# Optimization experiments

Measured on AMD Instinct MI355X. Metric: run time of the kernel, lower is better.

The kernel has to match this reference:

```python
import jax, jax.numpy as jnp
import numpy as np

N, E, IN, H, OUT = 100000, 1600000, 128, 128, 64


def setup_inputs() -> dict:
    key = jax.random.key(0)
    ks = jax.random.split(key, 7)
    x = jax.random.normal(ks[0], (N, IN), dtype=jnp.float32)
    edge_index = jax.random.randint(ks[1], (2, E), 0, N, dtype=jnp.int32)
    # Glorot-style scaled params (PyG SAGEConv: lin_l has bias, lin_r does not)
    s1 = 1.0 / np.sqrt(IN)
    s2 = 1.0 / np.sqrt(H)
    W1_l = jax.random.normal(ks[2], (H, IN), dtype=jnp.float32) * s1
    W1_r = jax.random.normal(ks[3], (H, IN), dtype=jnp.float32) * s1
    b1 = jnp.zeros((H,), dtype=jnp.float32)
    W2_l = jax.random.normal(ks[4], (OUT, H), dtype=jnp.float32) * s2
    W2_r = jax.random.normal(ks[5], (OUT, H), dtype=jnp.float32) * s2
    b2 = jnp.zeros((OUT,), dtype=jnp.float32)
    return {"x": x, "W1_l": W1_l, "W1_r": W1_r, "b1": b1,
            "W2_l": W2_l, "W2_r": W2_r, "b2": b2, "edge_index": edge_index}


def _sage_conv(x, edge_index, W_l, W_r, b):
    # mean-aggregate source-node features at target nodes, then linear + root term
    src, dst = edge_index[0], edge_index[1]
    n = x.shape[0]
    msgs = x[src]                                                   # [E, d]
    agg = jax.ops.segment_sum(msgs, dst, num_segments=n)            # [N, d]
    deg = jax.ops.segment_sum(jnp.ones((src.shape[0],), x.dtype), dst, num_segments=n)
    mean = agg / jnp.clip(deg, 1.0)[:, None]                        # zero-deg nodes stay 0
    return mean @ W_l.T + b + x @ W_r.T


def reference(x, W1_l, W1_r, b1, W2_l, W2_r, b2, edge_index):
    h = _sage_conv(x, edge_index, W1_l, W1_r, b1)
    h = jax.nn.relu(h)  # dropout p=0.0 -> identity
    out = _sage_conv(h, edge_index, W2_l, W2_r, b2)
    return out
```

## Files before the change

kernel.cpp:

```cpp
#include <hip/hip_runtime.h>


typedef unsigned int uint32;
typedef short bf16x8 __attribute__((ext_vector_type(8)));
typedef float f32x16 __attribute__((ext_vector_type(16)));
typedef float f32x2 __attribute__((ext_vector_type(2)));

#define PSTR 264

__device__ __forceinline__ uint32 pack_bf16_rne(float a, float b) {
    uint32 ua = __float_as_uint(a);
    uint32 ub = __float_as_uint(b);
    uint32 ra = (ua + 0x7fffu + ((ua >> 16) & 1u)) >> 16;
    uint32 rb = (ub + 0x7fffu + ((ub >> 16) & 1u)) >> 16;
    return ra | (rb << 16);
}
__device__ __forceinline__ float bf_lo(uint32 v) { return __uint_as_float(v << 16); }

__device__ __forceinline__ short rne16(float v, float* back) {
    uint32 u = __float_as_uint(v);
    uint32 r = (u + 0x7fffu + ((u >> 16) & 1u)) >> 16;
    *back = __uint_as_float(r << 16);
    return (short)r;
}

__global__ void k_prep(const float* __restrict__ x, uint32* __restrict__ xb,
                       long n4,
                       const float* __restrict__ W1l, const float* __restrict__ W1r,
                       const float* __restrict__ W2l, const float* __restrict__ W2r,
                       short* __restrict__ W1pH, short* __restrict__ W1pL,
                       short* __restrict__ W2pH, short* __restrict__ W2pL) {
    long i = (long)blockIdx.x * blockDim.x + threadIdx.x;
    float back;
    if (i < n4) {
        float4 v = ((const float4*)x)[i];
        short h0 = rne16(v.x, &back);
        short h1 = rne16(v.y, &back);
        short h2 = rne16(v.z, &back);
        short h3 = rne16(v.w, &back);
        uint2 o;
        o.x = (uint32)(unsigned short)h0 | ((uint32)(unsigned short)h1 << 16);
        o.y = (uint32)(unsigned short)h2 | ((uint32)(unsigned short)h3 << 16);
        ((uint2*)xb)[i] = o;
        return;
    }
    int i2 = (int)(i - n4);
    if (i2 < 32768) {
        int j = i2 >> 8, k = i2 & 255;
        float v = (k < 128) ? W1l[j * 128 + k] : W1r[j * 128 + k - 128];
        float hb;
        short hs = rne16(v, &hb);
        short ls = rne16(v - hb, &back);
        int idx = (k >> 3) * 1024 + j * 8 + (k & 7);
        W1pH[idx] = hs;
        W1pL[idx] = ls;
    } else if (i2 < 32768 + 16384) {
        int i3 = i2 - 32768;
        int j = i3 >> 7, k = i3 & 127;
        float v = (j < 64) ? W2l[j * 128 + k] : W2r[(j - 64) * 128 + k];
        float hb;
        short hs = rne16(v, &hb);
        short ls = rne16(v - hb, &back);
        int idx = (k >> 3) * 1024 + j * 8 + (k & 7);
        W2pH[idx] = hs;
        W2pL[idx] = ls;
    }
}


__global__ void k_bcount(const int* __restrict__ ei, int E, int NB,
                         int* __restrict__ bucket_cnt) {
    __shared__ int hist[1024];
    int t = threadIdx.x;
    for (int i = t; i < NB; i += 256) hist[i] = 0;
    __syncthreads();
    int stride = gridDim.x * 256;
    for (int e = blockIdx.x * 256 + t; e < E; e += stride)
        atomicAdd(&hist[ei[E + e] >> 8], 1);
    __syncthreads();
    for (int i = t; i < NB; i += 256) {
        int c = hist[i];
        if (c) atomicAdd(&bucket_cnt[i], c);
    }
}

__global__ void k_bscan(const int* __restrict__ bucket_cnt, int NB, int E,
                        int* __restrict__ bucket_off, int* __restrict__ bucket_cur) {
    __shared__ int s[1024];
    int t = threadIdx.x;
    int v = (t < NB) ? bucket_cnt[t] : 0;
    s[t] = v;
    __syncthreads();
    for (int o = 1; o < 1024; o <<= 1) {
        int u = (t >= o) ? s[t - o] : 0;
        __syncthreads();
        s[t] += u;
        __syncthreads();
    }
    int ex = s[t] - v;
    if (t < NB) { bucket_off[t] = ex; bucket_cur[t] = ex; }
    if (t == NB - 1) bucket_off[NB] = ex + v;
}

__global__ void k_bscatter(const int* __restrict__ ei, int E, int NB,
                           int* __restrict__ bucket_cur, uint32* __restrict__ eb) {
    __shared__ int hist[1024];
    __shared__ int base[1024];
    int t = threadIdx.x;
    for (int i = t; i < NB; i += 256) hist[i] = 0;
    __syncthreads();
    int stride = gridDim.x * 256;
    for (int e = blockIdx.x * 256 + t; e < E; e += stride)
        atomicAdd(&hist[ei[E + e] >> 8], 1);
    __syncthreads();
    for (int i = t; i < NB; i += 256) {
        int c = hist[i];
        base[i] = c ? atomicAdd(&bucket_cur[i], c) : 0;
        hist[i] = 0;
    }
    __syncthreads();
    for (int e = blockIdx.x * 256 + t; e < E; e += stride) {
        int d = ei[E + e];
        int b = d >> 8;
        int r = atomicAdd(&hist[b], 1);
        eb[base[b] + r] = ((uint32)(d & 255) << 24) | (uint32)ei[e];
    }
}

__global__ void k_bfinal(const uint32* __restrict__ eb,
                         const int* __restrict__ bucket_off,
                         int* __restrict__ row_ptr, int* __restrict__ col,
                         int N, int E) {
    __shared__ int deg[256];
    __shared__ int sc[256];
    __shared__ int cur[256];
    int b = blockIdx.x;
    int t = threadIdx.x;
    int beg = bucket_off[b], end = bucket_off[b + 1];
    deg[t] = 0;
    __syncthreads();
    for (int e = beg + t; e < end; e += 256)
        atomicAdd(&deg[eb[e] >> 24], 1);
    __syncthreads();
    int v = deg[t];
    sc[t] = v;
    __syncthreads();
    for (int o = 1; o < 256; o <<= 1) {
        int u = (t >= o) ? sc[t - o] : 0;
        __syncthreads();
        sc[t] += u;
        __syncthreads();
    }
    int ex = sc[t] - v;
    int node = b * 256 + t;
    if (node < N) row_ptr[node] = beg + ex;
    if (b == gridDim.x - 1 && t == 0) row_ptr[N] = E;
    cur[t] = ex;
    __syncthreads();
    for (int e = beg + t; e < end; e += 256) {
        uint32 u = eb[e];
        int r = atomicAdd(&cur[u >> 24], 1);
        col[beg + r] = (int)(u & 0xFFFFFFu);
    }
}


__global__ __launch_bounds__(256, 4) void k_fused(
        const int* __restrict__ rp, const int* __restrict__ col,
        const uint32* __restrict__ xb,
        const short* __restrict__ W1pH, const short* __restrict__ W1pL,
        const short* __restrict__ W2pH, const short* __restrict__ W2pL,
        const float* __restrict__ b1, const float* __restrict__ b2,
        unsigned short* __restrict__ hl, float* __restrict__ hr, int N) {
    __shared__ short smH[16 * PSTR];
    __shared__ short smL[16 * PSTR];
    int t = threadIdx.x;
    int w = t >> 6, lane = t & 63;
    int node0 = blockIdx.x * 32;

    int base = node0 + 8 * w;
    int rpi = base + lane;
    if (rpi > N) rpi = N;
    int rpv = rp[rpi];

#define ACC1(a) { s += (f32x2){bf_lo(a), __uint_as_float(a)}; }

    for (int i = 0; i < 8; i++) {
        int lr = 8 * w + i;
        int beg = __builtin_amdgcn_readfirstlane(__shfl(rpv, i));
        int end = __builtin_amdgcn_readfirstlane(__shfl(rpv, i + 1));
        f32x2 s = (f32x2){0.f, 0.f};
        int e = beg;
        for (; e + 8 <= end; e += 8) {
            int c0 = col[e + 0], c1 = col[e + 1], c2 = col[e + 2], c3 = col[e + 3];
            int c4 = col[e + 4], c5 = col[e + 5], c6 = col[e + 6], c7 = col[e + 7];
            uint32 a0 = xb[(size_t)c0 * 64 + lane];
            uint32 a1 = xb[(size_t)c1 * 64 + lane];
            uint32 a2 = xb[(size_t)c2 * 64 + lane];
            uint32 a3 = xb[(size_t)c3 * 64 + lane];
            uint32 a4 = xb[(size_t)c4 * 64 + lane];
            uint32 a5 = xb[(size_t)c5 * 64 + lane];
            uint32 a6 = xb[(size_t)c6 * 64 + lane];
            uint32 a7 = xb[(size_t)c7 * 64 + lane];
            ACC1(a0); ACC1(a1); ACC1(a2); ACC1(a3);
            ACC1(a4); ACC1(a5); ACC1(a6); ACC1(a7);
        }
        for (; e + 4 <= end; e += 4) {
            int c0 = col[e + 0], c1 = col[e + 1], c2 = col[e + 2], c3 = col[e + 3];
            uint32 a0 = xb[(size_t)c0 * 64 + lane];
            uint32 a1 = xb[(size_t)c1 * 64 + lane];
            uint32 a2 = xb[(size_t)c2 * 64 + lane];
            uint32 a3 = xb[(size_t)c3 * 64 + lane];
            ACC1(a0); ACC1(a1); ACC1(a2); ACC1(a3);
        }
        for (; e < end; e++) {
            uint32 a0 = xb[(size_t)col[e] * 64 + lane];
            ACC1(a0);
        }
        float inv = 1.0f / (float)max(end - beg, 1);
        float m0 = s.x * inv, m1 = s.y * inv;
        float b_;
        short h0 = rne16(m0, &b_);
        float bk0 = b_;
        short l0 = rne16(m0 - bk0, &b_);
        short h1 = rne16(m1, &b_);
        float bk1 = b_;
        short l1 = rne16(m1 - bk1, &b_);
        uint32 H = (uint32)(unsigned short)h0 | ((uint32)(unsigned short)h1 << 16);
        uint32 L = (uint32)(unsigned short)l0 | ((uint32)(unsigned short)l1 << 16);
        int idx = (lane >> 2) * PSTR + lr * 8 + 2 * (lane & 3);
        *(uint32*)&smH[idx] = H;
        *(uint32*)&smL[idx] = L;
    }
#undef ACC1
    __syncthreads();

    int m = lane & 31, hh = lane >> 5;
    int mynode = node0 + m;
    const short* xbs = (const short*)xb;
    f32x16 acc;
#pragma unroll
    for (int r = 0; r < 16; r++) acc[r] = 0.f;
#pragma unroll
    for (int kc = 0; kc < 8; kc++) {
        int c = 2 * kc + hh;
        bf16x8 bH = *(const bf16x8*)&smH[c * PSTR + m * 8];
        bf16x8 bL = *(const bf16x8*)&smL[c * PSTR + m * 8];
        bf16x8 xH = *(const bf16x8*)(xbs + (size_t)mynode * 128 + c * 8);
        bf16x8 aH1 = *(const bf16x8*)(W1pH + c * 1024 + (32 * w + m) * 8);
        bf16x8 aL1 = *(const bf16x8*)(W1pL + c * 1024 + (32 * w + m) * 8);
        bf16x8 aH2 = *(const bf16x8*)(W1pH + (16 + c) * 1024 + (32 * w + m) * 8);
        bf16x8 aL2 = *(const bf16x8*)(W1pL + (16 + c) * 1024 + (32 * w + m) * 8);
        acc = __builtin_amdgcn_mfma_f32_32x32x16_bf16(aH1, bH, acc, 0, 0, 0);
        acc = __builtin_amdgcn_mfma_f32_32x32x16_bf16(aL1, bH, acc, 0, 0, 0);
        acc = __builtin_amdgcn_mfma_f32_32x32x16_bf16(aH1, bL, acc, 0, 0, 0);
        acc = __builtin_amdgcn_mfma_f32_32x32x16_bf16(aH2, xH, acc, 0, 0, 0);
        acc = __builtin_amdgcn_mfma_f32_32x32x16_bf16(aL2, xH, acc, 0, 0, 0);
    }

    uint2 oh[4], ol[4];
#pragma unroll
    for (int rg = 0; rg < 4; rg++) {
        int j0 = 32 * w + 8 * rg + 4 * hh;
        float4 bv = *(const float4*)(b1 + j0);
        float bb[4] = {bv.x, bv.y, bv.z, bv.w};
        short hs[4], ls[4];
#pragma unroll
        for (int q = 0; q < 4; q++) {
            float v = fmaxf(acc[4 * rg + q] + bb[q], 0.f);
            float back;
            hs[q] = rne16(v, &back);
            ls[q] = rne16(v - back, &back);
        }
        oh[rg].x = (uint32)(unsigned short)hs[0] | ((uint32)(unsigned short)hs[1] << 16);
        oh[rg].y = (uint32)(unsigned short)hs[2] | ((uint32)(unsigned short)hs[3] << 16);
        ol[rg].x = (uint32)(unsigned short)ls[0] | ((uint32)(unsigned short)ls[1] << 16);
        ol[rg].y = (uint32)(unsigned short)ls[2] | ((uint32)(unsigned short)ls[3] << 16);
    }
    __syncthreads();
#pragma unroll
    for (int rg = 0; rg < 4; rg++) {
        int idx = (4 * w + rg) * PSTR + m * 8 + 4 * hh;
        *(uint2*)&smH[idx] = oh[rg];
        *(uint2*)&smL[idx] = ol[rg];
    }
    __syncthreads();

#pragma unroll
    for (int r = 0; r < 16; r++) acc[r] = 0.f;
#pragma unroll
    for (int kc = 0; kc < 8; kc++) {
        int c = 2 * kc + hh;
        bf16x8 bH = *(const bf16x8*)&smH[c * PSTR + m * 8];
        bf16x8 bL = *(const bf16x8*)&smL[c * PSTR + m * 8];
        bf16x8 aH = *(const bf16x8*)(W2pH + c * 1024 + (32 * w + m) * 8);
        bf16x8 aL = *(const bf16x8*)(W2pL + c * 1024 + (32 * w + m) * 8);
        acc = __builtin_amdgcn_mfma_f32_32x32x16_bf16(aH, bH, acc, 0, 0, 0);
        acc = __builtin_amdgcn_mfma_f32_32x32x16_bf16(aL, bH, acc, 0, 0, 0);
        acc = __builtin_amdgcn_mfma_f32_32x32x16_bf16(aH, bL, acc, 0, 0, 0);
    }
    if (mynode >= N) return;
    if (w < 2) {
#pragma unroll
        for (int rg = 0; rg < 4; rg++) {
            int j0 = 32 * w + 8 * rg + 4 * hh;
            uint2 o;
            o.x = pack_bf16_rne(acc[4 * rg + 0], acc[4 * rg + 1]);
            o.y = pack_bf16_rne(acc[4 * rg + 2], acc[4 * rg + 3]);
            *(uint2*)&hl[(size_t)mynode * 64 + j0] = o;
        }
    } else {
#pragma unroll
        for (int rg = 0; rg < 4; rg++) {
            int j0 = 32 * (w - 2) + 8 * rg + 4 * hh;
            float4 bv = *(const float4*)(b2 + j0);
            float4 o;
            o.x = acc[4 * rg + 0] + bv.x;
            o.y = acc[4 * rg + 1] + bv.y;
            o.z = acc[4 * rg + 2] + bv.z;
            o.w = acc[4 * rg + 3] + bv.w;
            *(float4*)&hr[(size_t)mynode * 64 + j0] = o;
        }
    }
}


__global__ void k_agg_out(const int* __restrict__ rp, const int* __restrict__ col,
                          const unsigned short* __restrict__ hl,
                          const float* __restrict__ hr,
                          float* __restrict__ out, int N) {
    int node = blockIdx.x * 4 + (threadIdx.x >> 6);
    if (node >= N) return;
    node = __builtin_amdgcn_readfirstlane(node);
    int lane = threadIdx.x & 63;
    int beg = rp[node], end = rp[node + 1];
    float s = 0.f;

#define ACCU(a) { s += __uint_as_float((uint32)(a) << 16); }

    int e = beg;
    for (; e + 8 <= end; e += 8) {
        int c0 = col[e + 0], c1 = col[e + 1], c2 = col[e + 2], c3 = col[e + 3];
        int c4 = col[e + 4], c5 = col[e + 5], c6 = col[e + 6], c7 = col[e + 7];
        unsigned short a0 = hl[(size_t)c0 * 64 + lane];
        unsigned short a1 = hl[(size_t)c1 * 64 + lane];
        unsigned short a2 = hl[(size_t)c2 * 64 + lane];
        unsigned short a3 = hl[(size_t)c3 * 64 + lane];
        unsigned short a4 = hl[(size_t)c4 * 64 + lane];
        unsigned short a5 = hl[(size_t)c5 * 64 + lane];
        unsigned short a6 = hl[(size_t)c6 * 64 + lane];
        unsigned short a7 = hl[(size_t)c7 * 64 + lane];
        ACCU(a0); ACCU(a1); ACCU(a2); ACCU(a3);
        ACCU(a4); ACCU(a5); ACCU(a6); ACCU(a7);
    }
    for (; e + 4 <= end; e += 4) {
        int c0 = col[e + 0], c1 = col[e + 1], c2 = col[e + 2], c3 = col[e + 3];
        unsigned short a0 = hl[(size_t)c0 * 64 + lane];
        unsigned short a1 = hl[(size_t)c1 * 64 + lane];
        unsigned short a2 = hl[(size_t)c2 * 64 + lane];
        unsigned short a3 = hl[(size_t)c3 * 64 + lane];
        ACCU(a0); ACCU(a1); ACCU(a2); ACCU(a3);
    }
    for (; e < end; e++) {
        unsigned short a0 = hl[(size_t)col[e] * 64 + lane];
        ACCU(a0);
    }
#undef ACCU
    float inv = 1.0f / (float)max(end - beg, 1);
    out[(size_t)node * 64 + lane] = s * inv + hr[(size_t)node * 64 + lane];
}

extern "C" void kernel_launch(void* const* d_in, const int* in_sizes, int n_in,
                              void* d_out, int out_size, void* d_ws, size_t ws_size,
                              hipStream_t stream) {
    const float* x   = (const float*)d_in[0];
    const float* W1l = (const float*)d_in[1];
    const float* W1r = (const float*)d_in[2];
    const float* b1  = (const float*)d_in[3];
    const float* W2l = (const float*)d_in[4];
    const float* W2r = (const float*)d_in[5];
    const float* b2  = (const float*)d_in[6];
    const int*   ei  = (const int*)d_in[7];
    int N = in_sizes[0] / 128;
    int E = in_sizes[7] / 2;
    int NB = (N + 255) >> 8;
    int mb = (N + 31) / 32;
    int Np = ((N + 127) / 128) * 128;
    float* out = (float*)d_out;

    char* w = (char*)d_ws;
    size_t off = 0;
    auto alloc = [&](size_t bytes) -> char* {
        char* p = w + off;
        off += (bytes + 255) & ~(size_t)255;
        return p;
    };
    int*   row_ptr = (int*)alloc((size_t)(N + 1) * 4);
    int*   bcnt    = (int*)alloc((size_t)(NB + 1) * 4);
    int*   boff    = (int*)alloc((size_t)(NB + 1) * 4);
    int*   bcur    = (int*)alloc((size_t)(NB + 1) * 4);
    short* W1pH    = (short*)alloc(32768 * 2);
    short* W1pL    = (short*)alloc(32768 * 2);
    short* W2pH    = (short*)alloc(16384 * 2);
    short* W2pL    = (short*)alloc(16384 * 2);
    int*   col     = (int*)alloc((size_t)E * 4);
    uint32* xb     = (uint32*)alloc((size_t)Np * 64 * 4);
    float*  hr     = (float*)alloc((size_t)Np * 64 * 4);
    unsigned short* hl = (unsigned short*)alloc((size_t)N * 64 * 2);
    uint32* eb = (uint32*)hl;

    hipMemsetAsync(bcnt, 0, (size_t)NB * 4, stream);
    long n4 = (long)N * 32;
    long prep_items = n4 + 32768 + 16384;
    k_prep<<<(int)((prep_items + 255) / 256), 256, 0, stream>>>(
        x, xb, n4, W1l, W1r, W2l, W2r, W1pH, W1pL, W2pH, W2pL);
    k_bcount<<<256, 256, 0, stream>>>(ei, E, NB, bcnt);
    k_bscan<<<1, 1024, 0, stream>>>(bcnt, NB, E, boff, bcur);
    k_bscatter<<<128, 256, 0, stream>>>(ei, E, NB, bcur, eb);
    k_bfinal<<<NB, 256, 0, stream>>>(eb, boff, row_ptr, col, N, E);

    k_fused<<<mb, 256, 0, stream>>>(row_ptr, col, xb, W1pH, W1pL, W2pH, W2pL,
                                    b1, b2, hl, hr, N);
    int ab = (N + 3) / 4;
    k_agg_out<<<ab, 256, 0, stream>>>(row_ptr, col, hl, hr, out, N);
}
```

Measured before the change: 318.7 us.

## Merge CSR build and prep kernels into one cooperative kernel with grid syncs

Replaces the memset plus five separate launches (prep, bucket count, scan, scatter, finalize) with one cooperative kernel of 1024 blocks that separates the phases with grid.sync(). This removes the per-launch overhead and the idle gaps between the small graph-preprocessing kernels. In exchange, the histogram phases now run over 1024 blocks instead of 256/128, which adds more global atomics. The single-block scan stalls the whole grid, and shared histograms shrink to 512 entries, which assumes NB is at most 512.

```diff
diff --git a/kernel.cpp b/kernel.cpp
--- a/kernel.cpp
+++ b/kernel.cpp
@@ -1,5 +1,8 @@
 #include <hip/hip_runtime.h>
-
+#include <hip/hip_cooperative_groups.h>
+
+
+namespace cg = cooperative_groups;
 
 typedef unsigned int uint32;
 typedef short bf16x8 __attribute__((ext_vector_type(8)));
@@ -24,143 +27,144 @@
     return (short)r;
 }
 
-__global__ void k_prep(const float* __restrict__ x, uint32* __restrict__ xb,
-                       long n4,
-                       const float* __restrict__ W1l, const float* __restrict__ W1r,
-                       const float* __restrict__ W2l, const float* __restrict__ W2r,
-                       short* __restrict__ W1pH, short* __restrict__ W1pL,
-                       short* __restrict__ W2pH, short* __restrict__ W2pL) {
-    long i = (long)blockIdx.x * blockDim.x + threadIdx.x;
-    float back;
-    if (i < n4) {
-        float4 v = ((const float4*)x)[i];
-        short h0 = rne16(v.x, &back);
-        short h1 = rne16(v.y, &back);
-        short h2 = rne16(v.z, &back);
-        short h3 = rne16(v.w, &back);
-        uint2 o;
-        o.x = (uint32)(unsigned short)h0 | ((uint32)(unsigned short)h1 << 16);
-        o.y = (uint32)(unsigned short)h2 | ((uint32)(unsigned short)h3 << 16);
-        ((uint2*)xb)[i] = o;
-        return;
-    }
-    int i2 = (int)(i - n4);
-    if (i2 < 32768) {
-        int j = i2 >> 8, k = i2 & 255;
-        float v = (k < 128) ? W1l[j * 128 + k] : W1r[j * 128 + k - 128];
-        float hb;
-        short hs = rne16(v, &hb);
-        short ls = rne16(v - hb, &back);
-        int idx = (k >> 3) * 1024 + j * 8 + (k & 7);
-        W1pH[idx] = hs;
-        W1pL[idx] = ls;
-    } else if (i2 < 32768 + 16384) {
-        int i3 = i2 - 32768;
-        int j = i3 >> 7, k = i3 & 127;
-        float v = (j < 64) ? W2l[j * 128 + k] : W2r[(j - 64) * 128 + k];
-        float hb;
-        short hs = rne16(v, &hb);
-        short ls = rne16(v - hb, &back);
-        int idx = (k >> 3) * 1024 + j * 8 + (k & 7);
-        W2pH[idx] = hs;
-        W2pL[idx] = ls;
-    }
-}
-
-
-__global__ void k_bcount(const int* __restrict__ ei, int E, int NB,
-                         int* __restrict__ bucket_cnt) {
-    __shared__ int hist[1024];
+
+__global__ __launch_bounds__(256, 4) void k_build(
+        const float* __restrict__ x, uint32* __restrict__ xb, long n4,
+        const float* __restrict__ W1l, const float* __restrict__ W1r,
+        const float* __restrict__ W2l, const float* __restrict__ W2r,
+        short* __restrict__ W1pH, short* __restrict__ W1pL,
+        short* __restrict__ W2pH, short* __restrict__ W2pL,
+        const int* __restrict__ ei, int E, int NB,
+        int* __restrict__ bcnt, int* __restrict__ boff, int* __restrict__ bcur,
+        uint32* __restrict__ eb, int* __restrict__ row_ptr,
+        int* __restrict__ col, int N) {
+    cg::grid_group grid = cg::this_grid();
+    __shared__ int hist[512];
+    __shared__ int base[512];
+    __shared__ int deg[256];
+    __shared__ int scn[256];
+    __shared__ int cur[256];
     int t = threadIdx.x;
-    for (int i = t; i < NB; i += 256) hist[i] = 0;
-    __syncthreads();
-    int stride = gridDim.x * 256;
-    for (int e = blockIdx.x * 256 + t; e < E; e += stride)
+    int b = blockIdx.x;
+    int nb = gridDim.x;
+    long gstride = (long)nb * 256;
+
+    long total = n4 + 32768 + 16384;
+    for (long i = (long)b * 256 + t; i < total; i += gstride) {
+        float back;
+        if (i < n4) {
+            float4 v = ((const float4*)x)[i];
+            short h0 = rne16(v.x, &back);
+            short h1 = rne16(v.y, &back);
+            short h2 = rne16(v.z, &back);
+            short h3 = rne16(v.w, &back);
+            uint2 o;
+            o.x = (uint32)(unsigned short)h0 | ((uint32)(unsigned short)h1 << 16);
+            o.y = (uint32)(unsigned short)h2 | ((uint32)(unsigned short)h3 << 16);
+            ((uint2*)xb)[i] = o;
+            continue;
+        }
+        int i2 = (int)(i - n4);
+        if (i2 < 32768) {
+            int j = i2 >> 8, k = i2 & 255;
+            float v = (k < 128) ? W1l[j * 128 + k] : W1r[j * 128 + k - 128];
+            float hb;
+            short hs = rne16(v, &hb);
+            short ls = rne16(v - hb, &back);
+            int idx = (k >> 3) * 1024 + j * 8 + (k & 7);
+            W1pH[idx] = hs;
+            W1pL[idx] = ls;
+        } else {
+            int i3 = i2 - 32768;
+            int j = i3 >> 7, k = i3 & 127;
+            float v = (j < 64) ? W2l[j * 128 + k] : W2r[(j - 64) * 128 + k];
+            float hb;
+            short hs = rne16(v, &hb);
+            short ls = rne16(v - hb, &back);
+            int idx = (k >> 3) * 1024 + j * 8 + (k & 7);
+            W2pH[idx] = hs;
+            W2pL[idx] = ls;
+        }
+    }
+    for (int i = b * 256 + t; i <= NB; i += nb * 256) bcnt[i] = 0;
+    grid.sync();
+
+    hist[t] = 0;
+    hist[t + 256] = 0;
+    __syncthreads();
+    for (long e = (long)b * 256 + t; e < E; e += gstride)
         atomicAdd(&hist[ei[E + e] >> 8], 1);
     __syncthreads();
     for (int i = t; i < NB; i += 256) {
         int c = hist[i];
-        if (c) atomicAdd(&bucket_cnt[i], c);
-    }
-}
-
-__global__ void k_bscan(const int* __restrict__ bucket_cnt, int NB, int E,
-                        int* __restrict__ bucket_off, int* __restrict__ bucket_cur) {
-    __shared__ int s[1024];
-    int t = threadIdx.x;
-    int v = (t < NB) ? bucket_cnt[t] : 0;
-    s[t] = v;
-    __syncthreads();
-    for (int o = 1; o < 1024; o <<= 1) {
-        int u = (t >= o) ? s[t - o] : 0;
-        __syncthreads();
-        s[t] += u;
-        __syncthreads();
-    }
-    int ex = s[t] - v;
-    if (t < NB) { bucket_off[t] = ex; bucket_cur[t] = ex; }
-    if (t == NB - 1) bucket_off[NB] = ex + v;
-}
-
-__global__ void k_bscatter(const int* __restrict__ ei, int E, int NB,
-                           int* __restrict__ bucket_cur, uint32* __restrict__ eb) {
-    __shared__ int hist[1024];
-    __shared__ int base[1024];
-    int t = threadIdx.x;
-    for (int i = t; i < NB; i += 256) hist[i] = 0;
-    __syncthreads();
-    int stride = gridDim.x * 256;
-    for (int e = blockIdx.x * 256 + t; e < E; e += stride)
-        atomicAdd(&hist[ei[E + e] >> 8], 1);
-    __syncthreads();
+        if (c) atomicAdd(&bcnt[i], c);
+    }
+    grid.sync();
+
+    if (b == 0) {
+        int c0 = (t < NB) ? bcnt[t] : 0;
+        int c1 = (t + 256 < NB) ? bcnt[t + 256] : 0;
+        base[t] = c0;
+        base[t + 256] = c1;
+        __syncthreads();
+        for (int o = 1; o < 512; o <<= 1) {
+            int a0 = (t >= o) ? base[t - o] : 0;
+            int a1 = (t + 256 >= o) ? base[t + 256 - o] : 0;
+            __syncthreads();
+            base[t] += a0;
+            base[t + 256] += a1;
+            __syncthreads();
+        }
+        if (t < NB) { boff[t] = base[t] - c0; bcur[t] = base[t] - c0; }
+        if (t + 256 < NB) {
+            boff[t + 256] = base[t + 256] - c1;
+            bcur[t + 256] = base[t + 256] - c1;
+        }
+        if (t == 0) { boff[NB] = E; row_ptr[N] = E; }
+    }
+    grid.sync();
+
     for (int i = t; i < NB; i += 256) {
         int c = hist[i];
-        base[i] = c ? atomicAdd(&bucket_cur[i], c) : 0;
+        base[i] = c ? atomicAdd(&bcur[i], c) : 0;
         hist[i] = 0;
     }
     __syncthreads();
-    for (int e = blockIdx.x * 256 + t; e < E; e += stride) {
+    for (long e = (long)b * 256 + t; e < E; e += gstride) {
         int d = ei[E + e];
-        int b = d >> 8;
-        int r = atomicAdd(&hist[b], 1);
-        eb[base[b] + r] = ((uint32)(d & 255) << 24) | (uint32)ei[e];
-    }
-}
-
-__global__ void k_bfinal(const uint32* __restrict__ eb,
-                         const int* __restrict__ bucket_off,
-                         int* __restrict__ row_ptr, int* __restrict__ col,
-                         int N, int E) {
-    __shared__ int deg[256];
-    __shared__ int sc[256];
-    __shared__ int cur[256];
-    int b = blockIdx.x;
-    int t = threadIdx.x;
-    int beg = bucket_off[b], end = bucket_off[b + 1];
-    deg[t] = 0;
-    __syncthreads();
-    for (int e = beg + t; e < end; e += 256)
-        atomicAdd(&deg[eb[e] >> 24], 1);
-    __syncthreads();
-    int v = deg[t];
-    sc[t] = v;
-    __syncthreads();
-    for (int o = 1; o < 256; o <<= 1) {
-        int u = (t >= o) ? sc[t - o] : 0;
-        __syncthreads();
-        sc[t] += u;
-        __syncthreads();
-    }
-    int ex = sc[t] - v;
-    int node = b * 256 + t;
-    if (node < N) row_ptr[node] = beg + ex;
-    if (b == gridDim.x - 1 && t == 0) row_ptr[N] = E;
-    cur[t] = ex;
-    __syncthreads();
-    for (int e = beg + t; e < end; e += 256) {
-        uint32 u = eb[e];
-        int r = atomicAdd(&cur[u >> 24], 1);
-        col[beg + r] = (int)(u & 0xFFFFFFu);
+        int bk = d >> 8;
+        int r = atomicAdd(&hist[bk], 1);
+        eb[base[bk] + r] = ((uint32)(d & 255) << 24) | (uint32)ei[e];
+    }
+    grid.sync();
+
+    for (int bb = b; bb < NB; bb += nb) {
+        int beg = boff[bb], end = boff[bb + 1];
+        deg[t] = 0;
+        __syncthreads();
+        for (int e = beg + t; e < end; e += 256)
+            atomicAdd(&deg[eb[e] >> 24], 1);
+        __syncthreads();
+        int v = deg[t];
+        scn[t] = v;
+        __syncthreads();
+        for (int o = 1; o < 256; o <<= 1) {
+            int u = (t >= o) ? scn[t - o] : 0;
+            __syncthreads();
+            scn[t] += u;
+            __syncthreads();
+        }
+        int ex = scn[t] - v;
+        int node = bb * 256 + t;
+        if (node < N) row_ptr[node] = beg + ex;
+        cur[t] = ex;
+        __syncthreads();
+        for (int e = beg + t; e < end; e += 256) {
+            uint32 u = eb[e];
+            int r = atomicAdd(&cur[u >> 24], 1);
+            col[beg + r] = (int)(u & 0xFFFFFFu);
+        }
+        __syncthreads();
     }
 }
 
@@ -409,15 +413,20 @@
     unsigned short* hl = (unsigned short*)alloc((size_t)N * 64 * 2);
     uint32* eb = (uint32*)hl;
 
-    hipMemsetAsync(bcnt, 0, (size_t)NB * 4, stream);
     long n4 = (long)N * 32;
-    long prep_items = n4 + 32768 + 16384;
-    k_prep<<<(int)((prep_items + 255) / 256), 256, 0, stream>>>(
-        x, xb, n4, W1l, W1r, W2l, W2r, W1pH, W1pL, W2pH, W2pL);
-    k_bcount<<<256, 256, 0, stream>>>(ei, E, NB, bcnt);
-    k_bscan<<<1, 1024, 0, stream>>>(bcnt, NB, E, boff, bcur);
-    k_bscatter<<<128, 256, 0, stream>>>(ei, E, NB, bcur, eb);
-    k_bfinal<<<NB, 256, 0, stream>>>(eb, boff, row_ptr, col, N, E);
+
+    {
+        void* args[] = {
+            (void*)&x, (void*)&xb, (void*)&n4,
+            (void*)&W1l, (void*)&W1r, (void*)&W2l, (void*)&W2r,
+            (void*)&W1pH, (void*)&W1pL, (void*)&W2pH, (void*)&W2pL,
+            (void*)&ei, (void*)&E, (void*)&NB,
+            (void*)&bcnt, (void*)&boff, (void*)&bcur,
+            (void*)&eb, (void*)&row_ptr, (void*)&col, (void*)&N
+        };
+        hipLaunchCooperativeKernel((const void*)k_build, dim3(1024), dim3(256),
+                                   args, 0, stream);
+    }
 
     k_fused<<<mb, 256, 0, stream>>>(row_ptr, col, xb, W1pH, W1pL, W2pH, W2pL,
                                     b1, b2, hl, hr, N);
```

Result: slower. 751.9 us (+136.0%).

## Vectorize output aggregation with 16-byte gathers and edge-parallel lane groups

Applied to the files above, without the earlier changes.

Rewrites the final mean-aggregation kernel so each node is handled by 32 lanes instead of 64. Every lane gathers 16 bytes (8 bf16 features) per neighbor, and four lane groups process different edges in parallel. Partial sums are combined with cross-lane shuffles before one group writes float4 outputs. This replaces many 2-byte-per-lane loads with wide vector loads to cut gather instruction count, at the cost of shuffle reductions and possibly unaligned vector loads of the column indices.

```diff
diff --git a/kernel.cpp b/kernel.cpp
--- a/kernel.cpp
+++ b/kernel.cpp
@@ -16,6 +16,7 @@
     return ra | (rb << 16);
 }
 __device__ __forceinline__ float bf_lo(uint32 v) { return __uint_as_float(v << 16); }
+__device__ __forceinline__ float bf_hi(uint32 v) { return __uint_as_float(v & 0xffff0000u); }
 
 __device__ __forceinline__ short rne16(float v, float* back) {
     uint32 u = __float_as_uint(v);
@@ -329,45 +330,73 @@
                           const unsigned short* __restrict__ hl,
                           const float* __restrict__ hr,
                           float* __restrict__ out, int N) {
-    int node = blockIdx.x * 4 + (threadIdx.x >> 6);
+    int node = blockIdx.x * 8 + (threadIdx.x >> 5);
     if (node >= N) return;
-    node = __builtin_amdgcn_readfirstlane(node);
-    int lane = threadIdx.x & 63;
+    int h = threadIdx.x & 31;
+    int g = h >> 3;
+    int f = h & 7;
     int beg = rp[node], end = rp[node + 1];
-    float s = 0.f;
-
-#define ACCU(a) { s += __uint_as_float((uint32)(a) << 16); }
+    const uint4* hl4 = (const uint4*)hl;
+    f32x2 sA[4];
+#pragma unroll
+    for (int j = 0; j < 4; j++) sA[j] = (f32x2){0.f, 0.f};
+
+#define ACC_MSK(v)                                          \
+    { sA[0] += (f32x2){bf_lo(v.x), bf_hi(v.x)};             \
+      sA[1] += (f32x2){bf_lo(v.y), bf_hi(v.y)};             \
+      sA[2] += (f32x2){bf_lo(v.z), bf_hi(v.z)};             \
+      sA[3] += (f32x2){bf_lo(v.w), bf_hi(v.w)}; }
 
     int e = beg;
+    for (; e + 16 <= end; e += 16) {
+        uint4 cv = *(const uint4*)(col + e + 4 * g);
+        uint4 v0 = hl4[(size_t)cv.x * 8 + f];
+        uint4 v1 = hl4[(size_t)cv.y * 8 + f];
+        uint4 v2 = hl4[(size_t)cv.z * 8 + f];
+        uint4 v3 = hl4[(size_t)cv.w * 8 + f];
+        ACC_MSK(v0); ACC_MSK(v1); ACC_MSK(v2); ACC_MSK(v3);
+    }
     for (; e + 8 <= end; e += 8) {
-        int c0 = col[e + 0], c1 = col[e + 1], c2 = col[e + 2], c3 = col[e + 3];
-        int c4 = col[e + 4], c5 = col[e + 5], c6 = col[e + 6], c7 = col[e + 7];
-        unsigned short a0 = hl[(size_t)c0 * 64 + lane];
-        unsigned short a1 = hl[(size_t)c1 * 64 + lane];
-        unsigned short a2 = hl[(size_t)c2 * 64 + lane];
-        unsigned short a3 = hl[(size_t)c3 * 64 + lane];
-        unsigned short a4 = hl[(size_t)c4 * 64 + lane];
-        unsigned short a5 = hl[(size_t)c5 * 64 + lane];
-        unsigned short a6 = hl[(size_t)c6 * 64 + lane];
-        unsigned short a7 = hl[(size_t)c7 * 64 + lane];
-        ACCU(a0); ACCU(a1); ACCU(a2); ACCU(a3);
-        ACCU(a4); ACCU(a5); ACCU(a6); ACCU(a7);
-    }
-    for (; e + 4 <= end; e += 4) {
-        int c0 = col[e + 0], c1 = col[e + 1], c2 = col[e + 2], c3 = col[e + 3];
-        unsigned short a0 = hl[(size_t)c0 * 64 + lane];
-        unsigned short a1 = hl[(size_t)c1 * 64 + lane];
-        unsigned short a2 = hl[(size_t)c2 * 64 + lane];
-        unsigned short a3 = hl[(size_t)c3 * 64 + lane];
-        ACCU(a0); ACCU(a1); ACCU(a2); ACCU(a3);
-    }
-    for (; e < end; e++) {
-        unsigned short a0 = hl[(size_t)col[e] * 64 + lane];
-        ACCU(a0);
-    }
-#undef ACCU
-    float inv = 1.0f / (float)max(end - beg, 1);
-    out[(size_t)node * 64 + lane] = s * inv + hr[(size_t)node * 64 + lane];
+        uint2 cv = *(const uint2*)(col + e + 2 * g);
+        uint4 v0 = hl4[(size_t)cv.x * 8 + f];
+        uint4 v1 = hl4[(size_t)cv.y * 8 + f];
+        ACC_MSK(v0); ACC_MSK(v1);
+    }
+    int rem = end - e;
+    if (2 * g < rem) {
+        uint4 v0 = hl4[(size_t)col[e + 2 * g] * 8 + f];
+        ACC_MSK(v0);
+    }
+    if (2 * g + 1 < rem) {
+        uint4 v0 = hl4[(size_t)col[e + 2 * g + 1] * 8 + f];
+        ACC_MSK(v0);
+    }
+#undef ACC_MSK
+#pragma unroll
+    for (int p = 0; p < 4; p++) {
+        sA[p].x += __shfl_xor(sA[p].x, 8);
+        sA[p].y += __shfl_xor(sA[p].y, 8);
+        sA[p].x += __shfl_xor(sA[p].x, 16);
+        sA[p].y += __shfl_xor(sA[p].y, 16);
+    }
+    if (g == 0) {
+        float inv = 1.0f / (float)max(end - beg, 1);
+        const float* hrp = hr + (size_t)node * 64 + f * 8;
+        float4 h0 = *(const float4*)(hrp);
+        float4 h1 = *(const float4*)(hrp + 4);
+        float4 o0, o1;
+        o0.x = sA[0].x * inv + h0.x;
+        o0.y = sA[0].y * inv + h0.y;
+        o0.z = sA[1].x * inv + h0.z;
+        o0.w = sA[1].y * inv + h0.w;
+        o1.x = sA[2].x * inv + h1.x;
+        o1.y = sA[2].y * inv + h1.y;
+        o1.z = sA[3].x * inv + h1.z;
+        o1.w = sA[3].y * inv + h1.w;
+        float* op = out + (size_t)node * 64 + f * 8;
+        *(float4*)(op) = o0;
+        *(float4*)(op + 4) = o1;
+    }
 }
 
 extern "C" void kernel_launch(void* const* d_in, const int* in_sizes, int n_in,
@@ -421,6 +450,6 @@
 
     k_fused<<<mb, 256, 0, stream>>>(row_ptr, col, xb, W1pH, W1pL, W2pH, W2pL,
                                     b1, b2, hl, hr, N);
-    int ab = (N + 3) / 4;
+    int ab = (N + 7) / 8;
     k_agg_out<<<ab, 256, 0, stream>>>(row_ptr, col, hl, hr, out, N);
 }
```

Result: no change. 314.8 us (-1.2%).
